# Kernel optimization log

Hardware: AMD Instinct MI355X
Metric: run time of the kernel (lower is better)

The kernel has to match this reference:

```python
import jax, jax.numpy as jnp
from jax import lax
import numpy as np

V, H = 512, 512


def gru_cell(x, h, Wih, Whh, bih, bhh):
    # PyTorch GRUCell: r,z,n gate order
    gi = x @ Wih.T + bih
    gh = h @ Whh.T + bhh
    ir, iz, inn = jnp.split(gi, 3, axis=-1)
    hr, hz, hn = jnp.split(gh, 3, axis=-1)
    r = jax.nn.sigmoid(ir + hr)
    z = jax.nn.sigmoid(iz + hz)
    n = jnp.tanh(inn + r * hn)
    return (1.0 - z) * n + z * h


def setup_inputs() -> dict:
    key = jax.random.key(0)
    ks = jax.random.split(key, 20)
    S, T, B = 200, 200, 256
    w = lambda k, shape: (jax.random.normal(k, shape, jnp.float32) * 0.05)
    inp = {
        "input_seq": jax.random.randint(ks[0], (S, B), 0, V),
        "input_len": jax.random.randint(ks[1], (B,), 1, S + 1),
        "target_seq": jax.random.randint(ks[2], (T, B), 0, V),
        "enc_embed": w(ks[3], (V, H)),
        "enc_Wih": w(ks[4], (3 * H, H)),
        "enc_Whh": w(ks[5], (3 * H, H)),
        "enc_bih": w(ks[6], (3 * H,)),
        "enc_bhh": w(ks[7], (3 * H,)),
        "att_W": w(ks[8], (H, H)),
        "att_b": w(ks[9], (H,)),
        "dec_embed": w(ks[10], (V, H)),
        "dec_Wih": w(ks[11], (3 * H, H)),
        "dec_Whh": w(ks[12], (3 * H, H)),
        "dec_bih": w(ks[13], (3 * H,)),
        "dec_bhh": w(ks[14], (3 * H,)),
        "mlp_W": w(ks[15], (H, 2 * H)),
        "mlp_b": w(ks[16], (H,)),
        "out_W": w(ks[17], (V, H)),
        "out_b": w(ks[18], (V,)),
    }
    return inp


def reference(input_seq, input_len, target_seq, enc_embed, enc_Wih, enc_Whh,
              enc_bih, enc_bhh, att_W, att_b, dec_embed, dec_Wih, dec_Whh,
              dec_bih, dec_bhh, mlp_W, mlp_b, out_W, out_b):
    S, B = input_seq.shape
    T = target_seq.shape[0]

    # ---- Encoder: length-masked GRU (equivalent to pack/pad) ----
    xs = enc_embed[input_seq]                              # (S,B,H)
    mask = jnp.arange(S)[:, None] < input_len[None, :]     # (S,B)
    h0 = jnp.zeros((B, H), xs.dtype)

    def estep(h, inp):
        x, m = inp
        m = m[:, None]
        hn = gru_cell(x, h, enc_Wih, enc_Whh, enc_bih, enc_bhh)
        h = jnp.where(m, hn, h)
        return h, jnp.where(m, h, 0.0)                     # padded outputs are zero

    h_enc, enc_out = lax.scan(estep, h0, (xs, mask))       # h_enc (B,H), enc_out (S,B,H)

    # ---- Decoder: teacher forcing (training path) ----
    dec_tokens = jnp.concatenate(
        [jnp.ones((1, B), target_seq.dtype), target_seq[:-1]], axis=0)  # start token 1
    dec_emb = dec_embed[dec_tokens]                        # (T,B,H)

    def dstep(h, emb_t):
        ah = jax.nn.relu(h @ att_W.T + att_b)              # (B,H)
        e = jnp.einsum('sbh,bh->bs', enc_out, ah)          # additive-style score
        att = jax.nn.softmax(e, axis=1)                    # (B,S)
        ctx = jnp.einsum('sbh,bs->bh', enc_out, att)       # (B,H)
        x = jnp.tanh(jnp.concatenate([emb_t, ctx], axis=1) @ mlp_W.T + mlp_b)
        hn = gru_cell(x, h, dec_Wih, dec_Whh, dec_bih, dec_bhh)
        dist = jax.nn.softmax(hn @ out_W.T + out_b, axis=1)
        return hn, dist

    _, dists = lax.scan(dstep, h_enc, dec_emb)             # (T,B,V)

    # ---- Loss: -log p[target] with clamp (== cal_loss) ----
    p = jnp.maximum(dists, 1e-10)
    tgt_p = jnp.take_along_axis(p, target_seq[:, :, None], axis=2)[..., 0]
    loss = jnp.mean(-jnp.log(tgt_p))

    # ---- Accuracy ----
    inference = jnp.argmax(dists, axis=-1)                 # (T,B)
    temacc = (inference == target_seq).astype(jnp.float32)
    all_acc = jnp.mean(temacc)
    acc = jnp.mean((jnp.sum(1.0 - temacc, axis=0) == 0).astype(jnp.float32))
    return inference.astype(jnp.float32), loss, acc, all_acc
```

## Files before the change

### kernel.cpp

```cpp
#include <hip/hip_runtime.h>
#include <math.h>

#define B 256
#define Hh 512
#define S 200
#define T 200
#define VOC 512
#define G3 1536
#define PAD 36

struct d4 { double x, y, z, w; };
__device__ __forceinline__ d4 tod4(const float4 a) {
    d4 r; r.x = a.x; r.y = a.y; r.z = a.z; r.w = a.w; return r;
}
__device__ __forceinline__ double dotd(const d4& a, const d4& b) {
    return a.x * b.x + a.y * b.y + a.z * b.z + a.w * b.w;
}
__device__ __forceinline__ double sigd(double x) { return 1.0 / (1.0 + exp(-x)); }

__global__ __launch_bounds__(256) void gemm_at(
    const float* __restrict__ A,
    const float* __restrict__ W, int ldw, int woff,
    const float* __restrict__ bias,
    float* __restrict__ C, int ldc)
{
    __shared__ float As[32][PAD];
    __shared__ float Ws[32][PAD];
    const int tid = threadIdx.x;
    const int tx = tid & 15, ty = tid >> 4;
    const int j0 = blockIdx.x * 32, m0 = blockIdx.y * 32;
    const int lr = tid >> 3, lc = (tid & 7) * 4;

    double acc00 = 0.0, acc01 = 0.0, acc10 = 0.0, acc11 = 0.0;

    for (int k0 = 0; k0 < 512; k0 += 32) {
        float4 av = *(const float4*)(A + (size_t)(m0 + lr) * 512 + k0 + lc);
        float4 wv = *(const float4*)(W + (size_t)(j0 + lr) * ldw + woff + k0 + lc);
        __syncthreads();
        *(float4*)&As[lr][lc] = av;
        *(float4*)&Ws[lr][lc] = wv;
        __syncthreads();
#pragma unroll
        for (int kk = 0; kk < 32; kk += 4) {
            d4 a0 = tod4(*(const float4*)&As[ty][kk]);
            d4 a1 = tod4(*(const float4*)&As[ty + 16][kk]);
            d4 b0 = tod4(*(const float4*)&Ws[tx][kk]);
            d4 b1 = tod4(*(const float4*)&Ws[tx + 16][kk]);
            acc00 += dotd(a0, b0);
            acc01 += dotd(a0, b1);
            acc10 += dotd(a1, b0);
            acc11 += dotd(a1, b1);
        }
    }
    const int ms[2] = { m0 + ty, m0 + ty + 16 };
    const int js[2] = { j0 + tx, j0 + tx + 16 };
    double accs[2][2] = { { acc00, acc01 }, { acc10, acc11 } };
#pragma unroll
    for (int mi = 0; mi < 2; ++mi)
#pragma unroll
        for (int ji = 0; ji < 2; ++ji) {
            int m = ms[mi], j = js[ji];
            C[(size_t)m * ldc + j] = (float)(accs[mi][ji] + (double)bias[j]);
        }
}

__global__ __launch_bounds__(512) void enc_step(
    const float* __restrict__ h_in, float* __restrict__ h_out,
    const float* __restrict__ gi_tab, const int* __restrict__ iseq,
    const int* __restrict__ ilen, const float* __restrict__ Whh,
    const float* __restrict__ bhh, int s, float* __restrict__ enc_out)
{
    __shared__ float Hs[32][68];
    __shared__ float Ws[48][68];
    const int tid = threadIdx.x;
    const int j_l = tid & 15, b_l = tid >> 4;
    const int j0 = blockIdx.x * 16, b0 = blockIdx.y * 32;
    const int j = j0 + j_l, b = b0 + b_l;

    int ml = 0;
    for (int i = 0; i < 32; ++i) ml = max(ml, ilen[b0 + i]);
    if (s >= ml) {
        h_out[(size_t)b * 512 + j] = h_in[(size_t)b * 512 + j];
        enc_out[((size_t)s * B + b) * 512 + j] = 0.f;
        return;
    }

    double ar = 0.0, az = 0.0, an = 0.0;
    for (int kt = 0; kt < 512; kt += 64) {
        __syncthreads();
        {
            int row = tid >> 4, c4 = (tid & 15) * 4;
            *(float4*)&Hs[row][c4] =
                *(const float4*)(h_in + (size_t)(b0 + row) * 512 + kt + c4);
            for (int idx = tid; idx < 768; idx += 512) {
                int r = idx >> 4, cc = (idx & 15) * 4;
                int g = r >> 4, jj = r & 15;
                *(float4*)&Ws[r][cc] =
                    *(const float4*)(Whh + (size_t)(g * 512 + j0 + jj) * 512 + kt + cc);
            }
        }
        __syncthreads();
#pragma unroll
        for (int kk = 0; kk < 64; kk += 4) {
            d4 hv = tod4(*(const float4*)&Hs[b_l][kk]);
            ar += dotd(hv, tod4(*(const float4*)&Ws[j_l][kk]));
            az += dotd(hv, tod4(*(const float4*)&Ws[16 + j_l][kk]));
            an += dotd(hv, tod4(*(const float4*)&Ws[32 + j_l][kk]));
        }
    }

    float hold = h_in[(size_t)b * 512 + j];
    float hnew = hold;
    if (s < ilen[b]) {
        int tok = iseq[s * B + b];
        const float* gi = gi_tab + (size_t)tok * G3;
        double r = sigd((double)gi[j] + ar + (double)bhh[j]);
        double z = sigd((double)gi[512 + j] + az + (double)bhh[512 + j]);
        double n = tanh((double)gi[1024 + j] + r * (an + (double)bhh[1024 + j]));
        hnew = (float)((1.0 - z) * n + z * (double)hold);
        enc_out[((size_t)s * B + b) * 512 + j] = hnew;
    } else {
        enc_out[((size_t)s * B + b) * 512 + j] = 0.f;
    }
    h_out[(size_t)b * 512 + j] = hnew;
}

__global__ __launch_bounds__(512) void proj(
    const float* __restrict__ h,
    const float* __restrict__ att_W, const float* __restrict__ att_b,
    const float* __restrict__ out_W, const float* __restrict__ out_b,
    float* __restrict__ ah, float* __restrict__ logits, int t)
{
    __shared__ float As[32][68];
    __shared__ float Ws[32][68];
    const int tid = threadIdx.x;
    const int tx = tid & 15, ty = tid >> 4;
    const int R0 = blockIdx.x * 32, m0 = blockIdx.y * 32;
    const bool is_att = (R0 < 512);
    if (is_att && t >= T) return;

    double a0 = 0.0, a1 = 0.0;
    for (int kt = 0; kt < 512; kt += 64) {
        __syncthreads();
        {
            int row = tid >> 4, c4 = (tid & 15) * 4;
            *(float4*)&As[row][c4] =
                *(const float4*)(h + (size_t)(m0 + row) * 512 + kt + c4);
            int R = R0 + row;
            const float* ws = is_att ? (att_W + (size_t)R * 512)
                                     : (out_W + (size_t)(R - 512) * 512);
            *(float4*)&Ws[row][c4] = *(const float4*)(ws + kt + c4);
        }
        __syncthreads();
#pragma unroll
        for (int kk = 0; kk < 64; kk += 4) {
            d4 av = tod4(*(const float4*)&As[ty][kk]);
            a0 += dotd(av, tod4(*(const float4*)&Ws[tx][kk]));
            a1 += dotd(av, tod4(*(const float4*)&Ws[16 + tx][kk]));
        }
    }

    const int m = m0 + ty;
    const int Ra = R0 + tx, Rb = R0 + tx + 16;
    if (is_att) {
        double v0 = a0 + (double)att_b[Ra]; if (v0 < 0.0) v0 = 0.0;
        double v1 = a1 + (double)att_b[Rb]; if (v1 < 0.0) v1 = 0.0;
        ah[(size_t)m * 512 + Ra] = (float)v0;
        ah[(size_t)m * 512 + Rb] = (float)v1;
    } else {
        logits[(size_t)m * 512 + (Ra - 512)] = (float)(a0 + (double)out_b[Ra - 512]);
        logits[(size_t)m * 512 + (Rb - 512)] = (float)(a1 + (double)out_b[Rb - 512]);
    }
}

__global__ __launch_bounds__(256) void attn_x_softmax(
    const float* __restrict__ enc_out, const float* __restrict__ ah,
    const float* __restrict__ mlp_W, const float* __restrict__ mlp_tab,
    const int* __restrict__ input_len, const int* __restrict__ target_seq,
    const float* __restrict__ logits, int t,
    float* __restrict__ xbuf, float* __restrict__ nll,
    float* __restrict__ inference)
{
    const int bid = blockIdx.x, tid = threadIdx.x;

    if (bid < B) {
        if (t >= T) return;
        __shared__ float scx[4][512];
        __shared__ double sml[8];
        __shared__ float ctxl[512];
        const int b = bid;
        const int wave = tid >> 6, lane = tid & 63;
        const int len = input_len[b];
        const float* ahb = ah + (size_t)b * 512;
        d4 aa1 = tod4(*(const float4*)(ahb + lane * 4));
        d4 aa2 = tod4(*(const float4*)(ahb + 256 + lane * 4));
        double m = -INFINITY, l = 0.0;
        d4 c1 = {0,0,0,0}, c2 = {0,0,0,0};
        for (int s = wave; s < len; s += 4) {
            const float* row = enc_out + ((size_t)s * B + b) * 512;
            d4 e1 = tod4(*(const float4*)(row + lane * 4));
            d4 e2 = tod4(*(const float4*)(row + 256 + lane * 4));
            double p = dotd(e1, aa1) + dotd(e2, aa2);
#pragma unroll
            for (int off = 32; off >= 1; off >>= 1) p += __shfl_xor(p, off, 64);
            double mn = fmax(m, p);
            double sc = (m == mn) ? 1.0 : exp(m - mn);
            double w = exp(p - mn);
            l = l * sc + w;
            c1.x = c1.x * sc + w * e1.x; c1.y = c1.y * sc + w * e1.y;
            c1.z = c1.z * sc + w * e1.z; c1.w = c1.w * sc + w * e1.w;
            c2.x = c2.x * sc + w * e2.x; c2.y = c2.y * sc + w * e2.y;
            c2.z = c2.z * sc + w * e2.z; c2.w = c2.w * sc + w * e2.w;
            m = mn;
        }
        if (lane == 0) { sml[wave] = m; sml[4 + wave] = l; }
        *(float4*)&scx[wave][lane * 4] =
            make_float4((float)c1.x, (float)c1.y, (float)c1.z, (float)c1.w);
        *(float4*)&scx[wave][256 + lane * 4] =
            make_float4((float)c2.x, (float)c2.y, (float)c2.z, (float)c2.w);
        __syncthreads();
        double M = fmax(fmax(sml[0], sml[1]), fmax(sml[2], sml[3]));
        if (len < S) M = fmax(M, 0.0);
        double w0 = exp(sml[0] - M), w1x = exp(sml[1] - M);
        double w2x = exp(sml[2] - M), w3 = exp(sml[3] - M);
        double L = sml[4] * w0 + sml[5] * w1x + sml[6] * w2x + sml[7] * w3
                 + (double)(S - len) * exp(0.0 - M);
        for (int jj = tid; jj < 512; jj += 256) {
            double v = (double)scx[0][jj] * w0 + (double)scx[1][jj] * w1x
                     + (double)scx[2][jj] * w2x + (double)scx[3][jj] * w3;
            ctxl[jj] = (float)(v / L);
        }
        __syncthreads();

        const int tok = (t == 0) ? 1 : target_seq[(t - 1) * B + b];
        const int q = tid & 3;
        const int rbase = tid >> 2;
#pragma unroll
        for (int pass = 0; pass < 8; ++pass) {
            const int jr = pass * 64 + rbase;
            const float* wr = mlp_W + (size_t)jr * 1024 + 512;
            double a = 0.0;
            for (int k = q * 4; k < 512; k += 16) {
                a += dotd(tod4(*(const float4*)&ctxl[k]),
                          tod4(*(const float4*)(wr + k)));
            }
            a += __shfl_xor(a, 1, 64);
            a += __shfl_xor(a, 2, 64);
            if (q == 0)
                xbuf[(size_t)b * 512 + jr] =
                    (float)tanh((double)mlp_tab[(size_t)tok * 512 + jr] + a);
        }
    } else {
        if (t < 1) return;
        __shared__ float red_f[256];
        __shared__ double red_d[256];
        __shared__ int red_i[256];
        const int sb = bid - B;
        const float* lg = logits + (size_t)sb * 512;
        const float l0 = lg[tid], l1 = lg[256 + tid];
        red_f[tid] = fmaxf(l0, l1);
        __syncthreads();
        for (int off = 128; off > 0; off >>= 1) {
            if (tid < off) red_f[tid] = fmaxf(red_f[tid], red_f[tid + off]);
            __syncthreads();
        }
        const double mx = (double)red_f[0];
        __syncthreads();
        const double e0 = exp((double)l0 - mx), e1 = exp((double)l1 - mx);
        red_d[tid] = e0 + e1;
        __syncthreads();
        for (int off = 128; off > 0; off >>= 1) {
            if (tid < off) red_d[tid] += red_d[tid + off];
            __syncthreads();
        }
        const double Z = red_d[0];
        __syncthreads();
        const float p0 = (float)(e0 / Z), p1 = (float)(e1 / Z);
        float v; int idx;
        if (p0 >= p1) { v = p0; idx = tid; } else { v = p1; idx = 256 + tid; }
        red_f[tid] = v; red_i[tid] = idx;
        __syncthreads();
        for (int off = 128; off > 0; off >>= 1) {
            if (tid < off) {
                float ov = red_f[tid + off]; int oi = red_i[tid + off];
                if (ov > red_f[tid] || (ov == red_f[tid] && oi < red_i[tid])) {
                    red_f[tid] = ov; red_i[tid] = oi;
                }
            }
            __syncthreads();
        }
        if (tid == 0) {
            int tg = target_seq[(t - 1) * B + sb];
            float pt = (float)(exp((double)lg[tg] - mx) / Z);
            pt = fmaxf(pt, 1e-10f);
            nll[(t - 1) * B + sb] = (float)(-log((double)pt));
            inference[(t - 1) * B + sb] = (float)red_i[0];
        }
    }
}

__global__ __launch_bounds__(256) void dec_gru(
    const float* __restrict__ x, const float* __restrict__ h_in,
    const float* __restrict__ Wih, const float* __restrict__ Whh,
    const float* __restrict__ bih, const float* __restrict__ bhh,
    float* __restrict__ h_out)
{
    __shared__ float Xs[16][36];
    __shared__ float Hs2[16][36];
    __shared__ float Wi[48][36];
    __shared__ float Wh[48][36];
    const int tid = threadIdx.x;
    const int j_l = tid & 15, b_l = tid >> 4;
    const int j0 = blockIdx.x * 16, b0 = blockIdx.y * 16;
    const int j = j0 + j_l, b = b0 + b_l;

    double air = 0, aiz = 0, ain = 0, ahr = 0, ahz = 0, ahn = 0;
    for (int kt = 0; kt < 512; kt += 32) {
        __syncthreads();
        for (int idx = tid; idx < 1024; idx += 256) {
            if (idx < 128) {
                int row = idx >> 3, c4 = (idx & 7) * 4;
                *(float4*)&Xs[row][c4] =
                    *(const float4*)(x + (size_t)(b0 + row) * 512 + kt + c4);
            } else if (idx < 256) {
                int w = idx - 128; int row = w >> 3, c4 = (w & 7) * 4;
                *(float4*)&Hs2[row][c4] =
                    *(const float4*)(h_in + (size_t)(b0 + row) * 512 + kt + c4);
            } else if (idx < 640) {
                int w = idx - 256; int row = w >> 3, c4 = (w & 7) * 4;
                int g = row >> 4, jj = row & 15;
                *(float4*)&Wi[row][c4] =
                    *(const float4*)(Wih + (size_t)(g * 512 + j0 + jj) * 512 + kt + c4);
            } else {
                int w = idx - 640; int row = w >> 3, c4 = (w & 7) * 4;
                int g = row >> 4, jj = row & 15;
                *(float4*)&Wh[row][c4] =
                    *(const float4*)(Whh + (size_t)(g * 512 + j0 + jj) * 512 + kt + c4);
            }
        }
        __syncthreads();
#pragma unroll
        for (int kk = 0; kk < 32; kk += 4) {
            d4 xv = tod4(*(const float4*)&Xs[b_l][kk]);
            d4 hv = tod4(*(const float4*)&Hs2[b_l][kk]);
            air += dotd(xv, tod4(*(const float4*)&Wi[j_l][kk]));
            aiz += dotd(xv, tod4(*(const float4*)&Wi[16 + j_l][kk]));
            ain += dotd(xv, tod4(*(const float4*)&Wi[32 + j_l][kk]));
            ahr += dotd(hv, tod4(*(const float4*)&Wh[j_l][kk]));
            ahz += dotd(hv, tod4(*(const float4*)&Wh[16 + j_l][kk]));
            ahn += dotd(hv, tod4(*(const float4*)&Wh[32 + j_l][kk]));
        }
    }

    double r = sigd(air + (double)bih[j] + ahr + (double)bhh[j]);
    double z = sigd(aiz + (double)bih[512 + j] + ahz + (double)bhh[512 + j]);
    double n = tanh(ain + (double)bih[1024 + j] + r * (ahn + (double)bhh[1024 + j]));
    float hold = h_in[(size_t)b * 512 + j];
    h_out[(size_t)b * 512 + j] = (float)((1.0 - z) * n + z * (double)hold);
}

__global__ __launch_bounds__(256) void finalize_k(
    const float* __restrict__ nll, const float* __restrict__ inference,
    const int* __restrict__ target, float* __restrict__ out3)
{
    const int tid = threadIdx.x;
    int wrong = 0;
    double match = 0.0;
    const int b = tid;
    for (int t = 0; t < T; ++t) {
        float inf = inference[t * B + b];
        float tg = (float)target[t * B + b];
        bool ok = (inf == tg);
        match += ok ? 1.0 : 0.0;
        wrong |= !ok;
    }
    double lsum = 0.0;
    for (int i = tid; i < T * B; i += 256) lsum += (double)nll[i];

    __shared__ double sl[256], sm_[256], sa[256];
    sl[tid] = lsum; sm_[tid] = match; sa[tid] = wrong ? 0.0 : 1.0;
    __syncthreads();
    for (int off = 128; off > 0; off >>= 1) {
        if (tid < off) {
            sl[tid] += sl[tid + off];
            sm_[tid] += sm_[tid + off];
            sa[tid] += sa[tid + off];
        }
        __syncthreads();
    }
    if (tid == 0) {
        out3[0] = (float)(sl[0] / (double)(T * B));
        out3[1] = (float)(sa[0] / (double)B);
        out3[2] = (float)(sm_[0] / (double)(T * B));
    }
}

extern "C" void kernel_launch(void* const* d_in, const int* in_sizes, int n_in,
                              void* d_out, int out_size, void* d_ws, size_t ws_size,
                              hipStream_t stream)
{
    const int*   input_seq  = (const int*)d_in[0];
    const int*   input_len  = (const int*)d_in[1];
    const int*   target_seq = (const int*)d_in[2];
    const float* enc_embed  = (const float*)d_in[3];
    const float* enc_Wih    = (const float*)d_in[4];
    const float* enc_Whh    = (const float*)d_in[5];
    const float* enc_bih    = (const float*)d_in[6];
    const float* enc_bhh    = (const float*)d_in[7];
    const float* att_W      = (const float*)d_in[8];
    const float* att_b      = (const float*)d_in[9];
    const float* dec_embed  = (const float*)d_in[10];
    const float* dec_Wih    = (const float*)d_in[11];
    const float* dec_Whh    = (const float*)d_in[12];
    const float* dec_bih    = (const float*)d_in[13];
    const float* dec_bhh    = (const float*)d_in[14];
    const float* mlp_W      = (const float*)d_in[15];
    const float* mlp_b      = (const float*)d_in[16];
    const float* out_W      = (const float*)d_in[17];
    const float* out_b      = (const float*)d_in[18];

    float* out = (float*)d_out;

    float* gi_tab  = (float*)d_ws;
    float* mlp_tab = gi_tab + (size_t)VOC * G3;
    float* h0      = mlp_tab + (size_t)VOC * Hh;
    float* h1      = h0 + (size_t)B * Hh;
    float* ahb     = h1 + (size_t)B * Hh;
    float* xb      = ahb + (size_t)B * Hh;
    float* lgb     = xb + (size_t)B * Hh;
    float* nllb    = lgb + (size_t)B * Hh;
    float* enc_out = nllb + (size_t)T * B;

    hipMemsetAsync(h0, 0, (size_t)B * Hh * sizeof(float), stream);

    gemm_at<<<dim3(48, 16), 256, 0, stream>>>(
        enc_embed, enc_Wih, 512, 0, enc_bih, gi_tab, G3);
    gemm_at<<<dim3(16, 16), 256, 0, stream>>>(
        dec_embed, mlp_W, 1024, 0, mlp_b, mlp_tab, Hh);

    for (int s = 0; s < S; ++s) {
        const float* hc = (s & 1) ? h1 : h0;
        float* hx = (s & 1) ? h0 : h1;
        enc_step<<<dim3(32, 8), 512, 0, stream>>>(
            hc, hx, gi_tab, input_seq, input_len, enc_Whh, enc_bhh, s, enc_out);
    }

    for (int t = 0; t <= T; ++t) {
        const float* hc = (t & 1) ? h1 : h0;
        float* hx = (t & 1) ? h0 : h1;
        proj<<<dim3(32, 8), 512, 0, stream>>>(
            hc, att_W, att_b, out_W, out_b, ahb, lgb, t);
        attn_x_softmax<<<dim3(2 * B), 256, 0, stream>>>(
            enc_out, ahb, mlp_W, mlp_tab, input_len, target_seq,
            lgb, t, xb, nllb, out);
        if (t < T) {
            dec_gru<<<dim3(32, 16), 256, 0, stream>>>(
                xb, hc, dec_Wih, dec_Whh, dec_bih, dec_bhh, hx);
        }
    }

    finalize_k<<<dim3(1), 256, 0, stream>>>(nllb, out, target_seq, out + (size_t)T * B);
}
```

Before: 33.18 ms.

## Fuse decoder projections into attention kernel and drop LDS tiling in GRU steps

The separate proj kernel (att_W and out_W matvecs) is folded into the per-batch attention/softmax kernel, which cuts one launch per decoder step and the ah/logits round trips through global memory. The encoder and decoder GRU step kernels lose their shared-memory tiling and read weights and states straight from global/L2. dec_gru also handles two batch rows per thread and launches half as many blocks. In exchange, each block now recomputes its matvec with only 256 threads, and the direct global loads lose the LDS reuse, so performance depends on cache behaviour and the extra per-block serial work.

```diff
diff --git a/kernel.cpp b/kernel.cpp
--- a/kernel.cpp
+++ b/kernel.cpp
@@ -70,43 +70,29 @@
     const int* __restrict__ ilen, const float* __restrict__ Whh,
     const float* __restrict__ bhh, int s, float* __restrict__ enc_out)
 {
-    __shared__ float Hs[32][68];
-    __shared__ float Ws[48][68];
     const int tid = threadIdx.x;
-    const int j_l = tid & 15, b_l = tid >> 4;
-    const int j0 = blockIdx.x * 16, b0 = blockIdx.y * 32;
-    const int j = j0 + j_l, b = b0 + b_l;
+    const int j = blockIdx.x * 16 + (tid & 15);
+    const int b = blockIdx.y * 32 + (tid >> 4);
 
     int ml = 0;
-    for (int i = 0; i < 32; ++i) ml = max(ml, ilen[b0 + i]);
+    for (int i = 0; i < 32; ++i) ml = max(ml, ilen[blockIdx.y * 32 + i]);
     if (s >= ml) {
         h_out[(size_t)b * 512 + j] = h_in[(size_t)b * 512 + j];
         enc_out[((size_t)s * B + b) * 512 + j] = 0.f;
         return;
     }
 
+    const float* hb = h_in + (size_t)b * 512;
+    const float* wr = Whh + (size_t)j * 512;
+    const float* wz = Whh + (size_t)(512 + j) * 512;
+    const float* wn = Whh + (size_t)(1024 + j) * 512;
     double ar = 0.0, az = 0.0, an = 0.0;
-    for (int kt = 0; kt < 512; kt += 64) {
-        __syncthreads();
-        {
-            int row = tid >> 4, c4 = (tid & 15) * 4;
-            *(float4*)&Hs[row][c4] =
-                *(const float4*)(h_in + (size_t)(b0 + row) * 512 + kt + c4);
-            for (int idx = tid; idx < 768; idx += 512) {
-                int r = idx >> 4, cc = (idx & 15) * 4;
-                int g = r >> 4, jj = r & 15;
-                *(float4*)&Ws[r][cc] =
-                    *(const float4*)(Whh + (size_t)(g * 512 + j0 + jj) * 512 + kt + cc);
-            }
-        }
-        __syncthreads();
-#pragma unroll
-        for (int kk = 0; kk < 64; kk += 4) {
-            d4 hv = tod4(*(const float4*)&Hs[b_l][kk]);
-            ar += dotd(hv, tod4(*(const float4*)&Ws[j_l][kk]));
-            az += dotd(hv, tod4(*(const float4*)&Ws[16 + j_l][kk]));
-            an += dotd(hv, tod4(*(const float4*)&Ws[32 + j_l][kk]));
-        }
+#pragma unroll 2
+    for (int k = 0; k < 512; k += 4) {
+        d4 hv = tod4(*(const float4*)(hb + k));
+        ar += dotd(hv, tod4(*(const float4*)(wr + k)));
+        az += dotd(hv, tod4(*(const float4*)(wz + k)));
+        an += dotd(hv, tod4(*(const float4*)(wn + k)));
     }
 
     float hold = h_in[(size_t)b * 512 + j];
@@ -125,75 +111,52 @@
     h_out[(size_t)b * 512 + j] = hnew;
 }
 
-__global__ __launch_bounds__(512) void proj(
-    const float* __restrict__ h,
+__global__ __launch_bounds__(256) void attn_ls(
+    const float* __restrict__ enc_out, const float* __restrict__ h,
     const float* __restrict__ att_W, const float* __restrict__ att_b,
     const float* __restrict__ out_W, const float* __restrict__ out_b,
-    float* __restrict__ ah, float* __restrict__ logits, int t)
-{
-    __shared__ float As[32][68];
-    __shared__ float Ws[32][68];
-    const int tid = threadIdx.x;
-    const int tx = tid & 15, ty = tid >> 4;
-    const int R0 = blockIdx.x * 32, m0 = blockIdx.y * 32;
-    const bool is_att = (R0 < 512);
-    if (is_att && t >= T) return;
-
-    double a0 = 0.0, a1 = 0.0;
-    for (int kt = 0; kt < 512; kt += 64) {
-        __syncthreads();
-        {
-            int row = tid >> 4, c4 = (tid & 15) * 4;
-            *(float4*)&As[row][c4] =
-                *(const float4*)(h + (size_t)(m0 + row) * 512 + kt + c4);
-            int R = R0 + row;
-            const float* ws = is_att ? (att_W + (size_t)R * 512)
-                                     : (out_W + (size_t)(R - 512) * 512);
-            *(float4*)&Ws[row][c4] = *(const float4*)(ws + kt + c4);
-        }
-        __syncthreads();
-#pragma unroll
-        for (int kk = 0; kk < 64; kk += 4) {
-            d4 av = tod4(*(const float4*)&As[ty][kk]);
-            a0 += dotd(av, tod4(*(const float4*)&Ws[tx][kk]));
-            a1 += dotd(av, tod4(*(const float4*)&Ws[16 + tx][kk]));
-        }
-    }
-
-    const int m = m0 + ty;
-    const int Ra = R0 + tx, Rb = R0 + tx + 16;
-    if (is_att) {
-        double v0 = a0 + (double)att_b[Ra]; if (v0 < 0.0) v0 = 0.0;
-        double v1 = a1 + (double)att_b[Rb]; if (v1 < 0.0) v1 = 0.0;
-        ah[(size_t)m * 512 + Ra] = (float)v0;
-        ah[(size_t)m * 512 + Rb] = (float)v1;
-    } else {
-        logits[(size_t)m * 512 + (Ra - 512)] = (float)(a0 + (double)out_b[Ra - 512]);
-        logits[(size_t)m * 512 + (Rb - 512)] = (float)(a1 + (double)out_b[Rb - 512]);
-    }
-}
-
-__global__ __launch_bounds__(256) void attn_x_softmax(
-    const float* __restrict__ enc_out, const float* __restrict__ ah,
     const float* __restrict__ mlp_W, const float* __restrict__ mlp_tab,
     const int* __restrict__ input_len, const int* __restrict__ target_seq,
-    const float* __restrict__ logits, int t,
-    float* __restrict__ xbuf, float* __restrict__ nll,
+    int t, float* __restrict__ xbuf, float* __restrict__ nll,
     float* __restrict__ inference)
 {
+    __shared__ float hl[512];
+    __shared__ float rowbuf[512];
+    __shared__ float scx[4][512];
+    __shared__ double sml[8];
+    __shared__ float ctxl[512];
+    __shared__ float red_f[256];
+    __shared__ double red_d[256];
+    __shared__ int red_i[256];
+
     const int bid = blockIdx.x, tid = threadIdx.x;
+    const int lane = tid & 63, wave = tid >> 6;
+    const int q = tid & 3, rbase = tid >> 2;
 
     if (bid < B) {
         if (t >= T) return;
-        __shared__ float scx[4][512];
-        __shared__ double sml[8];
-        __shared__ float ctxl[512];
         const int b = bid;
-        const int wave = tid >> 6, lane = tid & 63;
+        if (tid < 128) ((float4*)hl)[tid] = ((const float4*)(h + (size_t)b * 512))[tid];
+        __syncthreads();
+        for (int pass = 0; pass < 8; ++pass) {
+            const int jr = pass * 64 + rbase;
+            const float* wr = att_W + (size_t)jr * 512;
+            double a = 0.0;
+            for (int k = q * 4; k < 512; k += 16)
+                a += dotd(tod4(*(const float4*)(wr + k)),
+                          tod4(*(const float4*)&hl[k]));
+            a += __shfl_xor(a, 1, 64);
+            a += __shfl_xor(a, 2, 64);
+            if (q == 0) {
+                double v = a + (double)att_b[jr];
+                rowbuf[jr] = (float)(v > 0.0 ? v : 0.0);
+            }
+        }
+        __syncthreads();
+
         const int len = input_len[b];
-        const float* ahb = ah + (size_t)b * 512;
-        d4 aa1 = tod4(*(const float4*)(ahb + lane * 4));
-        d4 aa2 = tod4(*(const float4*)(ahb + 256 + lane * 4));
+        d4 aa1 = tod4(*(const float4*)&rowbuf[lane * 4]);
+        d4 aa2 = tod4(*(const float4*)&rowbuf[256 + lane * 4]);
         double m = -INFINITY, l = 0.0;
         d4 c1 = {0,0,0,0}, c2 = {0,0,0,0};
         for (int s = wave; s < len; s += 4) {
@@ -233,8 +196,6 @@
         __syncthreads();
 
         const int tok = (t == 0) ? 1 : target_seq[(t - 1) * B + b];
-        const int q = tid & 3;
-        const int rbase = tid >> 2;
 #pragma unroll
         for (int pass = 0; pass < 8; ++pass) {
             const int jr = pass * 64 + rbase;
@@ -252,12 +213,22 @@
         }
     } else {
         if (t < 1) return;
-        __shared__ float red_f[256];
-        __shared__ double red_d[256];
-        __shared__ int red_i[256];
         const int sb = bid - B;
-        const float* lg = logits + (size_t)sb * 512;
-        const float l0 = lg[tid], l1 = lg[256 + tid];
+        if (tid < 128) ((float4*)hl)[tid] = ((const float4*)(h + (size_t)sb * 512))[tid];
+        __syncthreads();
+        for (int pass = 0; pass < 8; ++pass) {
+            const int jr = pass * 64 + rbase;
+            const float* wr = out_W + (size_t)jr * 512;
+            double a = 0.0;
+            for (int k = q * 4; k < 512; k += 16)
+                a += dotd(tod4(*(const float4*)(wr + k)),
+                          tod4(*(const float4*)&hl[k]));
+            a += __shfl_xor(a, 1, 64);
+            a += __shfl_xor(a, 2, 64);
+            if (q == 0) rowbuf[jr] = (float)(a + (double)out_b[jr]);
+        }
+        __syncthreads();
+        const float l0 = rowbuf[tid], l1 = rowbuf[256 + tid];
         red_f[tid] = fmaxf(l0, l1);
         __syncthreads();
         for (int off = 128; off > 0; off >>= 1) {
@@ -291,7 +262,7 @@
         }
         if (tid == 0) {
             int tg = target_seq[(t - 1) * B + sb];
-            float pt = (float)(exp((double)lg[tg] - mx) / Z);
+            float pt = (float)(exp((double)rowbuf[tg] - mx) / Z);
             pt = fmaxf(pt, 1e-10f);
             nll[(t - 1) * B + sb] = (float)(-log((double)pt));
             inference[(t - 1) * B + sb] = (float)red_i[0];
@@ -305,58 +276,58 @@
     const float* __restrict__ bih, const float* __restrict__ bhh,
     float* __restrict__ h_out)
 {
-    __shared__ float Xs[16][36];
-    __shared__ float Hs2[16][36];
-    __shared__ float Wi[48][36];
-    __shared__ float Wh[48][36];
     const int tid = threadIdx.x;
-    const int j_l = tid & 15, b_l = tid >> 4;
-    const int j0 = blockIdx.x * 16, b0 = blockIdx.y * 16;
-    const int j = j0 + j_l, b = b0 + b_l;
-
-    double air = 0, aiz = 0, ain = 0, ahr = 0, ahz = 0, ahn = 0;
-    for (int kt = 0; kt < 512; kt += 32) {
-        __syncthreads();
-        for (int idx = tid; idx < 1024; idx += 256) {
-            if (idx < 128) {
-                int row = idx >> 3, c4 = (idx & 7) * 4;
-                *(float4*)&Xs[row][c4] =
-                    *(const float4*)(x + (size_t)(b0 + row) * 512 + kt + c4);
-            } else if (idx < 256) {
-                int w = idx - 128; int row = w >> 3, c4 = (w & 7) * 4;
-                *(float4*)&Hs2[row][c4] =
-                    *(const float4*)(h_in + (size_t)(b0 + row) * 512 + kt + c4);
-            } else if (idx < 640) {
-                int w = idx - 256; int row = w >> 3, c4 = (w & 7) * 4;
-                int g = row >> 4, jj = row & 15;
-                *(float4*)&Wi[row][c4] =
-                    *(const float4*)(Wih + (size_t)(g * 512 + j0 + jj) * 512 + kt + c4);
-            } else {
-                int w = idx - 640; int row = w >> 3, c4 = (w & 7) * 4;
-                int g = row >> 4, jj = row & 15;
-                *(float4*)&Wh[row][c4] =
-                    *(const float4*)(Whh + (size_t)(g * 512 + j0 + jj) * 512 + kt + c4);
-            }
-        }
-        __syncthreads();
-#pragma unroll
-        for (int kk = 0; kk < 32; kk += 4) {
-            d4 xv = tod4(*(const float4*)&Xs[b_l][kk]);
-            d4 hv = tod4(*(const float4*)&Hs2[b_l][kk]);
-            air += dotd(xv, tod4(*(const float4*)&Wi[j_l][kk]));
-            aiz += dotd(xv, tod4(*(const float4*)&Wi[16 + j_l][kk]));
-            ain += dotd(xv, tod4(*(const float4*)&Wi[32 + j_l][kk]));
-            ahr += dotd(hv, tod4(*(const float4*)&Wh[j_l][kk]));
-            ahz += dotd(hv, tod4(*(const float4*)&Wh[16 + j_l][kk]));
-            ahn += dotd(hv, tod4(*(const float4*)&Wh[32 + j_l][kk]));
-        }
-    }
-
-    double r = sigd(air + (double)bih[j] + ahr + (double)bhh[j]);
-    double z = sigd(aiz + (double)bih[512 + j] + ahz + (double)bhh[512 + j]);
-    double n = tanh(ain + (double)bih[1024 + j] + r * (ahn + (double)bhh[1024 + j]));
-    float hold = h_in[(size_t)b * 512 + j];
-    h_out[(size_t)b * 512 + j] = (float)((1.0 - z) * n + z * (double)hold);
+    const int j = blockIdx.x * 16 + (tid & 15);
+    const int b1 = blockIdx.y * 32 + (tid >> 4), b2 = b1 + 16;
+
+    const float* x1 = x + (size_t)b1 * 512;
+    const float* x2 = x + (size_t)b2 * 512;
+    const float* h1p = h_in + (size_t)b1 * 512;
+    const float* h2p = h_in + (size_t)b2 * 512;
+    const float* wir = Wih + (size_t)j * 512;
+    const float* wiz = Wih + (size_t)(512 + j) * 512;
+    const float* win = Wih + (size_t)(1024 + j) * 512;
+    const float* whr = Whh + (size_t)j * 512;
+    const float* whz = Whh + (size_t)(512 + j) * 512;
+    const float* whn = Whh + (size_t)(1024 + j) * 512;
+
+    double air1 = 0, aiz1 = 0, ain1 = 0, ahr1 = 0, ahz1 = 0, ahn1 = 0;
+    double air2 = 0, aiz2 = 0, ain2 = 0, ahr2 = 0, ahz2 = 0, ahn2 = 0;
+
+#pragma unroll 2
+    for (int k = 0; k < 512; k += 4) {
+        d4 vir = tod4(*(const float4*)(wir + k));
+        d4 viz = tod4(*(const float4*)(wiz + k));
+        d4 vin = tod4(*(const float4*)(win + k));
+        d4 vhr = tod4(*(const float4*)(whr + k));
+        d4 vhz = tod4(*(const float4*)(whz + k));
+        d4 vhn = tod4(*(const float4*)(whn + k));
+        d4 xv1 = tod4(*(const float4*)(x1 + k));
+        d4 hv1 = tod4(*(const float4*)(h1p + k));
+        d4 xv2 = tod4(*(const float4*)(x2 + k));
+        d4 hv2 = tod4(*(const float4*)(h2p + k));
+        air1 += dotd(xv1, vir); aiz1 += dotd(xv1, viz); ain1 += dotd(xv1, vin);
+        ahr1 += dotd(hv1, vhr); ahz1 += dotd(hv1, vhz); ahn1 += dotd(hv1, vhn);
+        air2 += dotd(xv2, vir); aiz2 += dotd(xv2, viz); ain2 += dotd(xv2, vin);
+        ahr2 += dotd(hv2, vhr); ahz2 += dotd(hv2, vhz); ahn2 += dotd(hv2, vhn);
+    }
+
+    const double bir = (double)bih[j], biz = (double)bih[512 + j], bin = (double)bih[1024 + j];
+    const double bhr = (double)bhh[j], bhz = (double)bhh[512 + j], bhn = (double)bhh[1024 + j];
+    {
+        double r = sigd(air1 + bir + ahr1 + bhr);
+        double z = sigd(aiz1 + biz + ahz1 + bhz);
+        double n = tanh(ain1 + bin + r * (ahn1 + bhn));
+        float hold = h_in[(size_t)b1 * 512 + j];
+        h_out[(size_t)b1 * 512 + j] = (float)((1.0 - z) * n + z * (double)hold);
+    }
+    {
+        double r = sigd(air2 + bir + ahr2 + bhr);
+        double z = sigd(aiz2 + biz + ahz2 + bhz);
+        double n = tanh(ain2 + bin + r * (ahn2 + bhn));
+        float hold = h_in[(size_t)b2 * 512 + j];
+        h_out[(size_t)b2 * 512 + j] = (float)((1.0 - z) * n + z * (double)hold);
+    }
 }
 
 __global__ __launch_bounds__(256) void finalize_k(
@@ -425,10 +396,8 @@
     float* mlp_tab = gi_tab + (size_t)VOC * G3;
     float* h0      = mlp_tab + (size_t)VOC * Hh;
     float* h1      = h0 + (size_t)B * Hh;
-    float* ahb     = h1 + (size_t)B * Hh;
-    float* xb      = ahb + (size_t)B * Hh;
-    float* lgb     = xb + (size_t)B * Hh;
-    float* nllb    = lgb + (size_t)B * Hh;
+    float* xb      = h1 + (size_t)B * Hh;
+    float* nllb    = xb + (size_t)B * Hh;
     float* enc_out = nllb + (size_t)T * B;
 
     hipMemsetAsync(h0, 0, (size_t)B * Hh * sizeof(float), stream);
@@ -448,13 +417,11 @@
     for (int t = 0; t <= T; ++t) {
         const float* hc = (t & 1) ? h1 : h0;
         float* hx = (t & 1) ? h0 : h1;
-        proj<<<dim3(32, 8), 512, 0, stream>>>(
-            hc, att_W, att_b, out_W, out_b, ahb, lgb, t);
-        attn_x_softmax<<<dim3(2 * B), 256, 0, stream>>>(
-            enc_out, ahb, mlp_W, mlp_tab, input_len, target_seq,
-            lgb, t, xb, nllb, out);
+        attn_ls<<<dim3(2 * B), 256, 0, stream>>>(
+            enc_out, hc, att_W, att_b, out_W, out_b, mlp_W, mlp_tab,
+            input_len, target_seq, t, xb, nllb, out);
         if (t < T) {
-            dec_gru<<<dim3(32, 16), 256, 0, stream>>>(
+            dec_gru<<<dim3(32, 8), 256, 0, stream>>>(
                 xb, hc, dec_Wih, dec_Whh, dec_bih, dec_bhh, hx);
         }
     }
```

New measurement: 63.26 ms. +90.7%, slower.
